# Optimization experiments

Measured on AMD Instinct MI355X. Metric: run time of the kernel, lower is better.

Reference implementation:

```python
import jax, jax.numpy as jnp
import numpy as np

D_MODEL = 1024
NUM_HEADS = 16
HEAD_DIM = D_MODEL // NUM_HEADS
SCALE = HEAD_DIM ** -0.5
LN_EPS = 1e-5
Q_EPS = 1e-5


def bit_quant(W):
    # BitNet b1.58 ternary weight quantization with straight-through estimator.
    gamma = jnp.mean(jnp.abs(W))
    Wq = jnp.clip(jnp.round(W / (gamma + Q_EPS)), -1.0, 1.0) * gamma
    return W + jax.lax.stop_gradient(Wq - W)


def layer_norm(x, gamma, beta):
    mu = jnp.mean(x, axis=-1, keepdims=True)
    var = jnp.mean(jnp.square(x - mu), axis=-1, keepdims=True)
    return (x - mu) * jax.lax.rsqrt(var + LN_EPS) * gamma + beta


def setup_inputs() -> dict:
    key = jax.random.key(0)
    ks = jax.random.split(key, 8)
    B, T, T_ctx, C = 4, 1024, 2048, D_MODEL
    w_std = C ** -0.5
    return {
        "x": jax.random.normal(ks[0], (B, T, C), jnp.float32),
        "context": jax.random.normal(ks[1], (B, T_ctx, C), jnp.float32),
        "Wq": jax.random.normal(ks[2], (C, C), jnp.float32) * w_std,
        "bq": jnp.zeros((C,), jnp.float32),
        "Wk": jax.random.normal(ks[3], (C, C), jnp.float32) * w_std,
        "bk": jnp.zeros((C,), jnp.float32),
        "Wv": jax.random.normal(ks[4], (C, C), jnp.float32) * w_std,
        "bv": jnp.zeros((C,), jnp.float32),
        "Wo": jax.random.normal(ks[5], (C, C), jnp.float32) * w_std,
        "bo": jnp.zeros((C,), jnp.float32),
        "ln_gamma": jnp.ones((C,), jnp.float32),
        "ln_beta": jnp.zeros((C,), jnp.float32),
    }


def reference(x, context, Wq, bq, Wk, bk, Wv, bv, Wo, bo, ln_gamma, ln_beta):
    B, T, C = x.shape
    T_ctx = context.shape[1]
    residual = x
    xn = layer_norm(x, ln_gamma, ln_beta)
    # BitNet-quantized projections (torch Linear: y = x @ W.T + b)
    q = xn @ bit_quant(Wq).T + bq                      # [B,T,C]
    k = context @ bit_quant(Wk).T + bk                 # [B,T_ctx,C]
    v = context @ bit_quant(Wv).T + bv                 # [B,T_ctx,C]
    q = q.reshape(B, T, NUM_HEADS, HEAD_DIM)
    k = k.reshape(B, T_ctx, NUM_HEADS, HEAD_DIM)
    v = v.reshape(B, T_ctx, NUM_HEADS, HEAD_DIM)
    scores = jnp.einsum("bqhd,bkhd->bhqk", q, k) * SCALE   # [B,H,T,T_ctx]
    probs = jax.nn.softmax(scores, axis=-1)
    out = jnp.einsum("bhqk,bkhd->bqhd", probs, v).reshape(B, T, C)
    return residual + (out @ bit_quant(Wo).T + bo)
```

## Files before the change

kernel.cpp:

```cpp
#include <hip/hip_runtime.h>
#include <hip/hip_bf16.h>

typedef __attribute__((ext_vector_type(8))) short s8x;
typedef __attribute__((ext_vector_type(4))) float f4x;
typedef unsigned short u16;
typedef unsigned int u32;

#define T_ 1024
#define TC_ 2048
#define SCLOG2E 0.1803368801111243f

__device__ __forceinline__ u16 f2bf(float f) {
    u32 u = __float_as_uint(f);
    return (u16)((u + 0x7fffu + ((u >> 16) & 1u)) >> 16);
}

#if defined(__has_builtin)
#if __has_builtin(__builtin_amdgcn_cvt_pk_bf16_f32)
#define HAVE_PK 1
#endif
#endif

__device__ __forceinline__ u32 pack2bf(float a, float b) {
#ifdef HAVE_PK
    typedef __attribute__((ext_vector_type(2))) __bf16 bf2t;
    bf2t r = __builtin_amdgcn_cvt_pk_bf16_f32(a, b);
    u32 u;
    __builtin_memcpy(&u, &r, 4);
    return u;
#else
    return (u32)f2bf(a) | ((u32)f2bf(b) << 16);
#endif
}

__device__ __forceinline__ void gload16(const void* g, void* l) {
    __builtin_amdgcn_global_load_lds((const __attribute__((address_space(1))) u32*)g,
                                     (__attribute__((address_space(3))) u32*)l, 16, 0, 0);
}

__global__ __launch_bounds__(256) void absmean_k(const float* __restrict__ W0, const float* __restrict__ W1,
                                                 const float* __restrict__ W2, const float* __restrict__ W3,
                                                 float* __restrict__ gsum) {
    int wi = blockIdx.y;
    const float* W = (wi == 0) ? W0 : (wi == 1) ? W1 : (wi == 2) ? W2 : W3;
    const int n4 = (1024 * 1024) / 4;
    float s = 0.f;
    int stride = gridDim.x * blockDim.x;
    for (int i = blockIdx.x * blockDim.x + threadIdx.x; i < n4; i += stride) {
        float4 v = ((const float4*)W)[i];
        s += fabsf(v.x) + fabsf(v.y) + fabsf(v.z) + fabsf(v.w);
    }
#pragma unroll
    for (int off = 32; off; off >>= 1) s += __shfl_down(s, off, 64);
    __shared__ float ps[4];
    if ((threadIdx.x & 63) == 0) ps[threadIdx.x >> 6] = s;
    __syncthreads();
    if (threadIdx.x == 0) atomicAdd(gsum + wi, ps[0] + ps[1] + ps[2] + ps[3]);
}

__global__ __launch_bounds__(256) void prep_k(
        const float* __restrict__ x, const float* __restrict__ lng, const float* __restrict__ lnb,
        u16* __restrict__ xn,
        const float* __restrict__ ctx, u16* __restrict__ ctxb,
        const float* __restrict__ W0, const float* __restrict__ W1,
        const float* __restrict__ W2, const float* __restrict__ W3,
        u16* __restrict__ D0, u16* __restrict__ D1, u16* __restrict__ D2, u16* __restrict__ D3,
        const float* __restrict__ gsum) {
    __shared__ float ps[8];
    int bx = blockIdx.x, t = threadIdx.x;
    if (bx < 4096) {
        int row = bx;
        float4 xv = ((const float4*)(x + (long)row * 1024))[t];
        float s = xv.x + xv.y + xv.z + xv.w;
        float s2 = xv.x * xv.x + xv.y * xv.y + xv.z * xv.z + xv.w * xv.w;
#pragma unroll
        for (int off = 32; off; off >>= 1) { s += __shfl_down(s, off, 64); s2 += __shfl_down(s2, off, 64); }
        if ((t & 63) == 0) { ps[t >> 6] = s; ps[4 + (t >> 6)] = s2; }
        __syncthreads();
        float S = ps[0] + ps[1] + ps[2] + ps[3];
        float S2 = ps[4] + ps[5] + ps[6] + ps[7];
        float mu = S * (1.f / 1024.f);
        float var = S2 * (1.f / 1024.f) - mu * mu;
        float rstd = rsqrtf(var + 1e-5f);
        float4 gv = ((const float4*)lng)[t];
        float4 bv = ((const float4*)lnb)[t];
        uint2 o;
        o.x = pack2bf((xv.x - mu) * rstd * gv.x + bv.x, (xv.y - mu) * rstd * gv.y + bv.y);
        o.y = pack2bf((xv.z - mu) * rstd * gv.z + bv.z, (xv.w - mu) * rstd * gv.w + bv.w);
        ((uint2*)(xn + (long)row * 1024))[t] = o;
    } else if (bx < 12288) {
        int i = (bx - 4096) * 256 + t;
        float4 v = ((const float4*)ctx)[i];
        uint2 o = {pack2bf(v.x, v.y), pack2bf(v.z, v.w)};
        ((uint2*)ctxb)[i] = o;
    } else {
        int wi = (bx - 12288) >> 10;
        const float* W = (wi == 0) ? W0 : (wi == 1) ? W1 : (wi == 2) ? W2 : W3;
        u16* D = (wi == 0) ? D0 : (wi == 1) ? D1 : (wi == 2) ? D2 : D3;
        float inv = 1.0f / (gsum[wi] * (1.0f / 1048576.0f) + 1e-5f);
        int i = ((bx - 12288) & 1023) * 256 + t;
        float4 wv = ((const float4*)W)[i];
        uint2 o;
        o.x = pack2bf(fminf(1.f, fmaxf(-1.f, rintf(wv.x * inv))),
                      fminf(1.f, fmaxf(-1.f, rintf(wv.y * inv))));
        o.y = pack2bf(fminf(1.f, fmaxf(-1.f, rintf(wv.z * inv))),
                      fminf(1.f, fmaxf(-1.f, rintf(wv.w * inv))));
        ((uint2*)D)[i] = o;
    }
}

__global__ __launch_bounds__(256) void gemm_fused(
        const u16* __restrict__ xn, const u16* __restrict__ ctxb,
        const u16* __restrict__ wtq, const u16* __restrict__ wtk, const u16* __restrict__ wtv,
        const float* __restrict__ bq, const float* __restrict__ bk, const float* __restrict__ bv,
        const float* __restrict__ gsum,
        u16* __restrict__ qb, u16* __restrict__ kb, u16* __restrict__ vtb) {
    __shared__ __align__(16) char smem[32768];
    int tid = threadIdx.x;
    int w = tid >> 6, l = tid & 63, lq = l & 15, lh = l >> 4;
    int wm = (w >> 1) * 64, wn = (w & 1) * 64;
    int bx = blockIdx.x;
    int xcd = bx & 7;
    int prob, m0, n0, gidx;
    const u16 *A, *Wt;
    const float* bias;
    float sc;
    if (bx < 256) {
        int local = bx >> 3;
        prob = 0; A = xn; Wt = wtq; bias = bq; sc = SCLOG2E; gidx = 0;
        m0 = (xcd * 4 + (local & 3)) * 128;
        n0 = (local >> 2) * 128;
    } else {
        int b = bx - 256;
        int local3 = b >> 3;
        int kv = local3 & 1;
        int idx = local3 >> 1;
        prob = 1 + kv; A = ctxb;
        Wt = kv ? wtv : wtk; bias = kv ? bv : bk; sc = 1.0f; gidx = 1 + kv;
        m0 = (xcd * 8 + (idx & 7)) * 128;
        n0 = (idx >> 3) * 128;
    }
    char* AsB = smem;
    char* BsB = smem + 16384;
    f4x acc[4][4] = {};
    int rb = tid >> 3;
    int cg = (tid & 7) ^ (rb & 7);
    const u16* Ag = A + (long)m0 * 1024 + cg * 8;
    const u16* Bg = Wt + (long)n0 * 1024 + cg * 8;
    for (int k0 = 0; k0 < 1024; k0 += 64) {
        __syncthreads();
#pragma unroll
        for (int i = 0; i < 4; i++) {
            gload16(Ag + (long)(i * 32 + rb) * 1024 + k0, AsB + (i * 256 + tid) * 16);
            gload16(Bg + (long)(i * 32 + rb) * 1024 + k0, BsB + (i * 256 + tid) * 16);
        }
        __syncthreads();
#pragma unroll
        for (int s = 0; s < 2; s++) {
            int sl = (s * 4 + lh) ^ (lq & 7);
            s8x af[4], bfr[4];
#pragma unroll
            for (int i = 0; i < 4; i++) {
                af[i] = *(const s8x*)(AsB + (wm + i * 16 + lq) * 128 + sl * 16);
                bfr[i] = *(const s8x*)(BsB + (wn + i * 16 + lq) * 128 + sl * 16);
            }
#pragma unroll
            for (int i = 0; i < 4; i++)
#pragma unroll
                for (int j = 0; j < 4; j++)
                    acc[i][j] = __builtin_amdgcn_mfma_f32_16x16x32_bf16(af[i], bfr[j], acc[i][j], 0, 0, 0);
        }
    }
    float gamma = gsum[gidx] * (1.0f / 1048576.0f) * sc;
    if (prob < 2) {
        u16* outq = (prob == 0) ? qb : kb;
        int tshift = (prob == 0) ? 10 : 11;
        int tmask = (1 << tshift) - 1;
#pragma unroll
        for (int i = 0; i < 4; i++) {
            int gr = m0 + wm + i * 16 + lh * 4;
#pragma unroll
            for (int j = 0; j < 4; j++) {
                int gc = n0 + wn + j * 16 + lq;
                float bb = bias[gc] * sc;
                int h = gc >> 6, d = gc & 63;
#pragma unroll
                for (int r = 0; r < 4; r++) {
                    int row = gr + r;
                    int bidx = row >> tshift, tt = row & tmask;
                    outq[((((long)(bidx * 16 + h)) << tshift) + tt) * 64 + d] = f2bf(acc[i][j][r] * gamma + bb);
                }
            }
        }
    } else {
        __syncthreads();
        char* Ct = smem;
#pragma unroll
        for (int i = 0; i < 4; i++) {
            int tt = wm + i * 16 + lh * 4;
#pragma unroll
            for (int j = 0; j < 4; j++) {
                int c = wn + j * 16 + lq;
                float bb = bias[n0 + c];
                uint2 pk;
                pk.x = pack2bf(acc[i][j][0] * gamma + bb, acc[i][j][1] * gamma + bb);
                pk.y = pack2bf(acc[i][j][2] * gamma + bb, acc[i][j][3] * gamma + bb);
                int slot = (tt >> 3) ^ (c & 15);
                *(uint2*)(Ct + c * 256 + slot * 16 + (tt & 7) * 2) = pk;
            }
        }
        __syncthreads();
        int bb2 = m0 >> 11, t0 = m0 & 2047;
#pragma unroll
        for (int it = 0; it < 8; it++) {
            int e = it * 256 + tid;
            int c = e >> 4, ch = e & 15;
            int slot = ch ^ (c & 15);
            s8x v = *(const s8x*)(Ct + c * 256 + slot * 16);
            int gcg = n0 + c;
            int h = gcg >> 6, d = gcg & 63;
            *(s8x*)(vtb + ((long)((bb2 * 16 + h) * 64 + d)) * TC_ + t0 + ch * 8) = v;
        }
    }
}

__global__ __launch_bounds__(256) void gemm_o(const u16* __restrict__ A, const u16* __restrict__ Wt,
                                              const float* __restrict__ bias, const float* __restrict__ gsum,
                                              const float* __restrict__ residual, float* __restrict__ outr) {
    __shared__ __align__(16) char smem[24576];
    int tid = threadIdx.x;
    int w = tid >> 6, l = tid & 63, lq = l & 15, lh = l >> 4;
    int wm = (w >> 1) * 64, wn = (w & 1) * 32;
    int bx = blockIdx.x;
    int xcd = bx & 7, local = bx >> 3;
    int m0 = (xcd * 4 + (local & 3)) * 128;
    int n0 = (local >> 2) * 64;
    char* AsB = smem;
    char* BsB = smem + 16384;
    f4x acc[4][2] = {};
    int rb = tid >> 3;
    int cg = (tid & 7) ^ (rb & 7);
    const u16* Ag = A + (long)m0 * 1024 + cg * 8;
    const u16* Bg = Wt + (long)n0 * 1024 + cg * 8;
    for (int k0 = 0; k0 < 1024; k0 += 64) {
        __syncthreads();
#pragma unroll
        for (int i = 0; i < 4; i++)
            gload16(Ag + (long)(i * 32 + rb) * 1024 + k0, AsB + (i * 256 + tid) * 16);
#pragma unroll
        for (int i = 0; i < 2; i++)
            gload16(Bg + (long)(i * 32 + rb) * 1024 + k0, BsB + (i * 256 + tid) * 16);
        __syncthreads();
#pragma unroll
        for (int s = 0; s < 2; s++) {
            int sl = (s * 4 + lh) ^ (lq & 7);
            s8x af[4], bfr[2];
#pragma unroll
            for (int i = 0; i < 4; i++)
                af[i] = *(const s8x*)(AsB + (wm + i * 16 + lq) * 128 + sl * 16);
#pragma unroll
            for (int j = 0; j < 2; j++)
                bfr[j] = *(const s8x*)(BsB + (wn + j * 16 + lq) * 128 + sl * 16);
#pragma unroll
            for (int i = 0; i < 4; i++)
#pragma unroll
                for (int j = 0; j < 2; j++)
                    acc[i][j] = __builtin_amdgcn_mfma_f32_16x16x32_bf16(af[i], bfr[j], acc[i][j], 0, 0, 0);
        }
    }
    float gamma = gsum[3] * (1.0f / 1048576.0f);
#pragma unroll
    for (int i = 0; i < 4; i++) {
        int gr = m0 + wm + i * 16 + lh * 4;
#pragma unroll
        for (int j = 0; j < 2; j++) {
            int gc = n0 + wn + j * 16 + lq;
            float bb = bias[gc];
#pragma unroll
            for (int r = 0; r < 4; r++) {
                long idx = (long)(gr + r) * 1024 + gc;
                outr[idx] = residual[idx] + acc[i][j][r] * gamma + bb;
            }
        }
    }
}

__global__ __launch_bounds__(512) void attn_k(const u16* __restrict__ qh, const u16* __restrict__ kh,
                                              const u16* __restrict__ vth,
                                              float* __restrict__ Opart, float* __restrict__ Mpart,
                                              float* __restrict__ Lpart) {
    __shared__ __align__(16) char smem[51200];
    int tid = threadIdx.x, w = tid >> 6, l = tid & 63, lq = l & 15, lh = l >> 4;
    int bh = blockIdx.x, q0 = blockIdx.y * 128, half = blockIdx.z;
    const u16* qp = qh + ((long)bh * T_ + q0) * 64;
    const u16* kp = kh + (long)bh * TC_ * 64 + half * 1024 * 64;
    const u16* vp = vth + (long)bh * 64 * TC_ + half * 1024;
#pragma unroll
    for (int i = 0; i < 2; i++) {
        int cid = i * 512 + tid;
        int r = cid >> 3, c = (cid & 7) ^ (r & 7);
        gload16(qp + r * 64 + c * 8, smem + cid * 16);
    }
    __syncthreads();
    s8x qf0, qf1;
    {
        int qrow = w * 16 + lq;
        qf0 = *(const s8x*)(smem + qrow * 128 + ((lh) ^ (qrow & 7)) * 16);
        qf1 = *(const s8x*)(smem + qrow * 128 + ((4 + lh) ^ (qrow & 7)) * 16);
    }
    __syncthreads();
#define STAGE_KV(kt, buf)                                                      \
    {                                                                          \
        char* Kb = smem + (buf) * 16384;                                       \
        char* Vb = Kb + 8192;                                                  \
        int r = tid >> 3, c = (tid & 7) ^ (r & 7);                             \
        gload16(kp + ((kt) * 64 + r) * 64 + c * 8, Kb + tid * 16);             \
        gload16(vp + (long)r * TC_ + (kt) * 64 + c * 8, Vb + tid * 16);        \
    }
    STAGE_KV(0, 0);
    f4x oacc[4] = {};
    f4x lrun = {};
    float mrun = -1e30f;
    const s8x ones = {16256, 16256, 16256, 16256, 16256, 16256, 16256, 16256};
    char* Psb = smem + 32768 + w * 2304;
    for (int kt = 0; kt < 16; kt++) {
        __syncthreads();
        if (kt + 1 < 16) STAGE_KV(kt + 1, (kt + 1) & 1);
        char* Ksb = smem + (kt & 1) * 16384;
        char* Vsb = Ksb + 8192;
        f4x z[4];
#pragma unroll
        for (int ni = 0; ni < 4; ni++) {
            int kr = ni * 16 + lq;
            s8x a0 = *(const s8x*)(Ksb + kr * 128 + ((lh) ^ (kr & 7)) * 16);
            s8x a1 = *(const s8x*)(Ksb + kr * 128 + ((4 + lh) ^ (kr & 7)) * 16);
            f4x zz = {0.f, 0.f, 0.f, 0.f};
            zz = __builtin_amdgcn_mfma_f32_16x16x32_bf16(a0, qf0, zz, 0, 0, 0);
            zz = __builtin_amdgcn_mfma_f32_16x16x32_bf16(a1, qf1, zz, 0, 0, 0);
            z[ni] = zz;
        }
        float mx = fmaxf(fmaxf(fmaxf(z[0][0], z[0][1]), fmaxf(z[0][2], z[0][3])),
                         fmaxf(fmaxf(z[1][0], z[1][1]), fmaxf(z[1][2], z[1][3])));
        mx = fmaxf(mx, fmaxf(fmaxf(fmaxf(z[2][0], z[2][1]), fmaxf(z[2][2], z[2][3])),
                             fmaxf(fmaxf(z[3][0], z[3][1]), fmaxf(z[3][2], z[3][3]))));
#pragma unroll
        for (int s = 1; s <= 32; s <<= 1) mx = fmaxf(mx, __shfl_xor(mx, s));
        float mn = fmaxf(mrun, mx);
        float al = __builtin_amdgcn_exp2f(mrun - mn);
        mrun = mn;
#pragma unroll
        for (int ni = 0; ni < 4; ni++) {
            uint2 pk;
            pk.x = pack2bf(__builtin_amdgcn_exp2f(z[ni][0] - mn), __builtin_amdgcn_exp2f(z[ni][1] - mn));
            pk.y = pack2bf(__builtin_amdgcn_exp2f(z[ni][2] - mn), __builtin_amdgcn_exp2f(z[ni][3] - mn));
            *(uint2*)(Psb + lq * 144 + ni * 32 + lh * 8) = pk;
        }
        if (al != 1.0f) {
#pragma unroll
            for (int nd = 0; nd < 4; nd++)
#pragma unroll
                for (int r = 0; r < 4; r++) oacc[nd][r] *= al;
#pragma unroll
            for (int r = 0; r < 4; r++) lrun[r] *= al;
        }
        s8x vf0[4], vf1[4];
#pragma unroll
        for (int nd = 0; nd < 4; nd++) {
            int vr = nd * 16 + lq;
            vf0[nd] = *(const s8x*)(Vsb + vr * 128 + ((lh) ^ (vr & 7)) * 16);
            vf1[nd] = *(const s8x*)(Vsb + vr * 128 + ((4 + lh) ^ (vr & 7)) * 16);
        }
        s8x pf0 = *(const s8x*)(Psb + lq * 144 + lh * 16);
        s8x pf1 = *(const s8x*)(Psb + lq * 144 + 64 + lh * 16);
        f4x rs = {0.f, 0.f, 0.f, 0.f};
        rs = __builtin_amdgcn_mfma_f32_16x16x32_bf16(pf0, ones, rs, 0, 0, 0);
        rs = __builtin_amdgcn_mfma_f32_16x16x32_bf16(pf1, ones, rs, 0, 0, 0);
#pragma unroll
        for (int r = 0; r < 4; r++) lrun[r] += rs[r];
#pragma unroll
        for (int nd = 0; nd < 4; nd++) {
            oacc[nd] = __builtin_amdgcn_mfma_f32_16x16x32_bf16(pf0, vf0[nd], oacc[nd], 0, 0, 0);
            oacc[nd] = __builtin_amdgcn_mfma_f32_16x16x32_bf16(pf1, vf1[nd], oacc[nd], 0, 0, 0);
        }
    }
    int pidx = (bh * 8 + blockIdx.y) * 2 + half;
    float* Op = Opart + (long)pidx * 8192;
#pragma unroll
    for (int r = 0; r < 4; r++) {
        int ql = w * 16 + lh * 4 + r;
#pragma unroll
        for (int nd = 0; nd < 4; nd++)
            Op[ql * 64 + nd * 16 + lq] = oacc[nd][r];
        if (lq == 0) Lpart[(long)pidx * 128 + ql] = lrun[r];
    }
    if (l == 0) Mpart[pidx * 8 + w] = mrun;
}

__global__ __launch_bounds__(256) void merge_k(const float* __restrict__ Opart,
                                               const float* __restrict__ Mpart,
                                               const float* __restrict__ Lpart,
                                               u16* __restrict__ attn) {
    int pg = blockIdx.x;
    int bh = pg >> 3, qt = pg & 7;
    int t = threadIdx.x;
    int q = t >> 1, dh = (t & 1) * 32;
    int p0 = pg * 2, p1 = pg * 2 + 1;
    float m0 = Mpart[p0 * 8 + (q >> 4)], m1 = Mpart[p1 * 8 + (q >> 4)];
    float l0 = Lpart[(long)p0 * 128 + q], l1 = Lpart[(long)p1 * 128 + q];
    float M = fmaxf(m0, m1);
    float a0 = __builtin_amdgcn_exp2f(m0 - M);
    float a1 = __builtin_amdgcn_exp2f(m1 - M);
    float rinv = 1.f / (l0 * a0 + l1 * a1);
    a0 *= rinv; a1 *= rinv;
    const float4* O0 = (const float4*)(Opart + (long)p0 * 8192 + q * 64 + dh);
    const float4* O1 = (const float4*)(Opart + (long)p1 * 8192 + q * 64 + dh);
    int b = bh >> 4, h = bh & 15;
    uint2* dst = (uint2*)(attn + ((long)(b * T_ + qt * 128 + q)) * 1024 + h * 64 + dh);
#pragma unroll
    for (int i = 0; i < 8; i++) {
        float4 v0 = O0[i], v1 = O1[i];
        uint2 o;
        o.x = pack2bf(v0.x * a0 + v1.x * a1, v0.y * a0 + v1.y * a1);
        o.y = pack2bf(v0.z * a0 + v1.z * a1, v0.w * a0 + v1.w * a1);
        dst[i] = o;
    }
}

extern "C" void kernel_launch(void* const* d_in, const int* in_sizes, int n_in,
                              void* d_out, int out_size, void* d_ws, size_t ws_size,
                              hipStream_t stream) {
    const float* x   = (const float*)d_in[0];
    const float* ctx = (const float*)d_in[1];
    const float* Wq  = (const float*)d_in[2];
    const float* bq  = (const float*)d_in[3];
    const float* Wk  = (const float*)d_in[4];
    const float* bk  = (const float*)d_in[5];
    const float* Wv  = (const float*)d_in[6];
    const float* bv  = (const float*)d_in[7];
    const float* Wo  = (const float*)d_in[8];
    const float* bo  = (const float*)d_in[9];
    const float* lng = (const float*)d_in[10];
    const float* lnb = (const float*)d_in[11];
    float* out = (float*)d_out;

    char* ws = (char*)d_ws;
    float* gsum = (float*)ws;
    size_t off = 256;
    u16* wtq  = (u16*)(ws + off); off += (size_t)1024 * 1024 * 2;
    u16* wtk  = (u16*)(ws + off); off += (size_t)1024 * 1024 * 2;
    u16* wtv  = (u16*)(ws + off); off += (size_t)1024 * 1024 * 2;
    u16* wto  = (u16*)(ws + off); off += (size_t)1024 * 1024 * 2;
    u16* ctxb = (u16*)(ws + off); off += (size_t)8192 * 1024 * 2;
    u16* xn   = (u16*)(ws + off); off += (size_t)4096 * 1024 * 2;
    u16* qb_  = (u16*)(ws + off); off += (size_t)4096 * 1024 * 2;
    u16* kb   = (u16*)(ws + off); off += (size_t)8192 * 1024 * 2;
    u16* vtb  = (u16*)(ws + off); off += (size_t)8192 * 1024 * 2;
    float* Opart = (float*)(ws + off); off += (size_t)1024 * 8192 * 4;
    float* Mpart = (float*)(ws + off); off += (size_t)1024 * 8 * 4;
    float* Lpart = (float*)(ws + off); off += (size_t)1024 * 128 * 4;
    u16* attnb = xn;

    hipMemsetAsync(gsum, 0, 16, stream);
    absmean_k<<<dim3(128, 4), 256, 0, stream>>>(Wq, Wk, Wv, Wo, gsum);
    prep_k<<<16384, 256, 0, stream>>>(x, lng, lnb, xn, ctx, ctxb,
                                      Wq, Wk, Wv, Wo, wtq, wtk, wtv, wto, gsum);
    gemm_fused<<<1280, 256, 0, stream>>>(xn, ctxb, wtq, wtk, wtv, bq, bk, bv, gsum, qb_, kb, vtb);
    attn_k<<<dim3(64, 8, 2), 512, 0, stream>>>(qb_, kb, vtb, Opart, Mpart, Lpart);
    merge_k<<<512, 256, 0, stream>>>(Opart, Mpart, Lpart, attnb);
    gemm_o<<<512, 256, 0, stream>>>(attnb, wto, bo, gsum, x, out);
}
```

Measured before the change: 282.6 us.

## Double-buffer GEMM k-loop with paired-row swizzle and store attention partials in bf16

Both projection GEMMs switch from a single-buffered 64-wide k step with two barriers per iteration to a double-buffered 32-wide k step. The next tile's global-to-LDS load is issued before the MFMAs on the current tile, leaving one barrier per step, and a new paired-row XOR swizzle with precomputed LDS offsets goes with it. Separately, the attention partial outputs are written as bf16 instead of fp32, which halves that traffic in attn_k and merge_k. The partial buffers now alias dead workspace regions (ctxb, wtq). This trades some precision in the partial sums for less bandwidth, and it relies on those aliased buffers no longer being needed.

```diff
diff --git a/kernel.cpp b/kernel.cpp
--- a/kernel.cpp
+++ b/kernel.cpp
@@ -10,6 +10,7 @@
 #define TC_ 2048
 #define SCLOG2E 0.1803368801111243f
 
+__device__ __forceinline__ float bf2f(u16 u) { return __uint_as_float(((u32)u) << 16); }
 __device__ __forceinline__ u16 f2bf(float f) {
     u32 u = __float_as_uint(f);
     return (u16)((u + 0x7fffu + ((u >> 16) & 1u)) >> 16);
@@ -140,36 +141,47 @@
         m0 = (xcd * 8 + (idx & 7)) * 128;
         n0 = (idx >> 3) * 128;
     }
-    char* AsB = smem;
-    char* BsB = smem + 16384;
+    int sp = tid >> 3, ss = tid & 7;
+    int st = ss ^ (sp & 7);
+    int r0 = sp * 2 + (st >> 2), c0 = st & 3;
+    const u16* Ag = A + (long)(m0 + r0) * 1024 + c0 * 8;
+    const u16* Bg = Wt + (long)(n0 + r0) * 1024 + c0 * 8;
+    int aoff[4], boff[4];
+#pragma unroll
+    for (int i = 0; i < 4; i++) {
+        int ar = wm + i * 16 + lq, ap = ar >> 1;
+        aoff[i] = ap * 128 + (((((ar & 1) << 2) | lh) ^ (ap & 7)) * 16);
+        int br = wn + i * 16 + lq, bp = br >> 1;
+        boff[i] = bp * 128 + (((((br & 1) << 2) | lh) ^ (bp & 7)) * 16);
+    }
     f4x acc[4][4] = {};
-    int rb = tid >> 3;
-    int cg = (tid & 7) ^ (rb & 7);
-    const u16* Ag = A + (long)m0 * 1024 + cg * 8;
-    const u16* Bg = Wt + (long)n0 * 1024 + cg * 8;
-    for (int k0 = 0; k0 < 1024; k0 += 64) {
-        __syncthreads();
+#define STAGE_G(kt, buf)                                                   \
+    {                                                                      \
+        char* Ad = smem + (buf) * 8192;                                    \
+        char* Bd = smem + 16384 + (buf) * 8192;                            \
+        int kk = (kt) * 32;                                                \
+        gload16(Ag + kk, Ad + tid * 16);                                   \
+        gload16(Ag + kk + 64 * 1024, Ad + 4096 + tid * 16);                \
+        gload16(Bg + kk, Bd + tid * 16);                                   \
+        gload16(Bg + kk + 64 * 1024, Bd + 4096 + tid * 16);                \
+    }
+    STAGE_G(0, 0);
+    for (int kt = 0; kt < 32; kt++) {
+        __syncthreads();
+        if (kt + 1 < 32) STAGE_G(kt + 1, (kt + 1) & 1);
+        const char* Ac = smem + (kt & 1) * 8192;
+        const char* Bc = smem + 16384 + (kt & 1) * 8192;
+        s8x af[4], bfr[4];
 #pragma unroll
         for (int i = 0; i < 4; i++) {
-            gload16(Ag + (long)(i * 32 + rb) * 1024 + k0, AsB + (i * 256 + tid) * 16);
-            gload16(Bg + (long)(i * 32 + rb) * 1024 + k0, BsB + (i * 256 + tid) * 16);
-        }
-        __syncthreads();
-#pragma unroll
-        for (int s = 0; s < 2; s++) {
-            int sl = (s * 4 + lh) ^ (lq & 7);
-            s8x af[4], bfr[4];
-#pragma unroll
-            for (int i = 0; i < 4; i++) {
-                af[i] = *(const s8x*)(AsB + (wm + i * 16 + lq) * 128 + sl * 16);
-                bfr[i] = *(const s8x*)(BsB + (wn + i * 16 + lq) * 128 + sl * 16);
-            }
-#pragma unroll
-            for (int i = 0; i < 4; i++)
-#pragma unroll
-                for (int j = 0; j < 4; j++)
-                    acc[i][j] = __builtin_amdgcn_mfma_f32_16x16x32_bf16(af[i], bfr[j], acc[i][j], 0, 0, 0);
-        }
+            af[i] = *(const s8x*)(Ac + aoff[i]);
+            bfr[i] = *(const s8x*)(Bc + boff[i]);
+        }
+#pragma unroll
+        for (int i = 0; i < 4; i++)
+#pragma unroll
+            for (int j = 0; j < 4; j++)
+                acc[i][j] = __builtin_amdgcn_mfma_f32_16x16x32_bf16(af[i], bfr[j], acc[i][j], 0, 0, 0);
     }
     float gamma = gsum[gidx] * (1.0f / 1048576.0f) * sc;
     if (prob < 2) {
@@ -235,38 +247,48 @@
     int xcd = bx & 7, local = bx >> 3;
     int m0 = (xcd * 4 + (local & 3)) * 128;
     int n0 = (local >> 2) * 64;
-    char* AsB = smem;
-    char* BsB = smem + 16384;
+    int sp = tid >> 3, ss = tid & 7;
+    int st = ss ^ (sp & 7);
+    int r0 = sp * 2 + (st >> 2), c0 = st & 3;
+    const u16* Ag = A + (long)(m0 + r0) * 1024 + c0 * 8;
+    const u16* Bg = Wt + (long)(n0 + r0) * 1024 + c0 * 8;
+    int aoff[4], boff[2];
+#pragma unroll
+    for (int i = 0; i < 4; i++) {
+        int ar = wm + i * 16 + lq, ap = ar >> 1;
+        aoff[i] = ap * 128 + (((((ar & 1) << 2) | lh) ^ (ap & 7)) * 16);
+    }
+#pragma unroll
+    for (int j = 0; j < 2; j++) {
+        int br = wn + j * 16 + lq, bp = br >> 1;
+        boff[j] = bp * 128 + (((((br & 1) << 2) | lh) ^ (bp & 7)) * 16);
+    }
     f4x acc[4][2] = {};
-    int rb = tid >> 3;
-    int cg = (tid & 7) ^ (rb & 7);
-    const u16* Ag = A + (long)m0 * 1024 + cg * 8;
-    const u16* Bg = Wt + (long)n0 * 1024 + cg * 8;
-    for (int k0 = 0; k0 < 1024; k0 += 64) {
-        __syncthreads();
+#define STAGE_O(kt, buf)                                                   \
+    {                                                                      \
+        char* Ad = smem + (buf) * 8192;                                    \
+        char* Bd = smem + 16384 + (buf) * 4096;                            \
+        int kk = (kt) * 32;                                                \
+        gload16(Ag + kk, Ad + tid * 16);                                   \
+        gload16(Ag + kk + 64 * 1024, Ad + 4096 + tid * 16);                \
+        gload16(Bg + kk, Bd + tid * 16);                                   \
+    }
+    STAGE_O(0, 0);
+    for (int kt = 0; kt < 32; kt++) {
+        __syncthreads();
+        if (kt + 1 < 32) STAGE_O(kt + 1, (kt + 1) & 1);
+        const char* Ac = smem + (kt & 1) * 8192;
+        const char* Bc = smem + 16384 + (kt & 1) * 4096;
+        s8x af[4], bfr[2];
+#pragma unroll
+        for (int i = 0; i < 4; i++) af[i] = *(const s8x*)(Ac + aoff[i]);
+#pragma unroll
+        for (int j = 0; j < 2; j++) bfr[j] = *(const s8x*)(Bc + boff[j]);
 #pragma unroll
         for (int i = 0; i < 4; i++)
-            gload16(Ag + (long)(i * 32 + rb) * 1024 + k0, AsB + (i * 256 + tid) * 16);
-#pragma unroll
-        for (int i = 0; i < 2; i++)
-            gload16(Bg + (long)(i * 32 + rb) * 1024 + k0, BsB + (i * 256 + tid) * 16);
-        __syncthreads();
-#pragma unroll
-        for (int s = 0; s < 2; s++) {
-            int sl = (s * 4 + lh) ^ (lq & 7);
-            s8x af[4], bfr[2];
-#pragma unroll
-            for (int i = 0; i < 4; i++)
-                af[i] = *(const s8x*)(AsB + (wm + i * 16 + lq) * 128 + sl * 16);
 #pragma unroll
             for (int j = 0; j < 2; j++)
-                bfr[j] = *(const s8x*)(BsB + (wn + j * 16 + lq) * 128 + sl * 16);
-#pragma unroll
-            for (int i = 0; i < 4; i++)
-#pragma unroll
-                for (int j = 0; j < 2; j++)
-                    acc[i][j] = __builtin_amdgcn_mfma_f32_16x16x32_bf16(af[i], bfr[j], acc[i][j], 0, 0, 0);
-        }
+                acc[i][j] = __builtin_amdgcn_mfma_f32_16x16x32_bf16(af[i], bfr[j], acc[i][j], 0, 0, 0);
     }
     float gamma = gsum[3] * (1.0f / 1048576.0f);
 #pragma unroll
@@ -287,7 +309,7 @@
 
 __global__ __launch_bounds__(512) void attn_k(const u16* __restrict__ qh, const u16* __restrict__ kh,
                                               const u16* __restrict__ vth,
-                                              float* __restrict__ Opart, float* __restrict__ Mpart,
+                                              u16* __restrict__ Opart, float* __restrict__ Mpart,
                                               float* __restrict__ Lpart) {
     __shared__ __align__(16) char smem[51200];
     int tid = threadIdx.x, w = tid >> 6, l = tid & 63, lq = l & 15, lh = l >> 4;
@@ -384,19 +406,19 @@
         }
     }
     int pidx = (bh * 8 + blockIdx.y) * 2 + half;
-    float* Op = Opart + (long)pidx * 8192;
+    u16* Op = Opart + (long)pidx * 8192;
 #pragma unroll
     for (int r = 0; r < 4; r++) {
         int ql = w * 16 + lh * 4 + r;
 #pragma unroll
         for (int nd = 0; nd < 4; nd++)
-            Op[ql * 64 + nd * 16 + lq] = oacc[nd][r];
+            Op[ql * 64 + nd * 16 + lq] = f2bf(oacc[nd][r]);
         if (lq == 0) Lpart[(long)pidx * 128 + ql] = lrun[r];
     }
     if (l == 0) Mpart[pidx * 8 + w] = mrun;
 }
 
-__global__ __launch_bounds__(256) void merge_k(const float* __restrict__ Opart,
+__global__ __launch_bounds__(256) void merge_k(const u16* __restrict__ Opart,
                                                const float* __restrict__ Mpart,
                                                const float* __restrict__ Lpart,
                                                u16* __restrict__ attn) {
@@ -412,16 +434,18 @@
     float a1 = __builtin_amdgcn_exp2f(m1 - M);
     float rinv = 1.f / (l0 * a0 + l1 * a1);
     a0 *= rinv; a1 *= rinv;
-    const float4* O0 = (const float4*)(Opart + (long)p0 * 8192 + q * 64 + dh);
-    const float4* O1 = (const float4*)(Opart + (long)p1 * 8192 + q * 64 + dh);
+    const uint2* O0 = (const uint2*)(Opart + (long)p0 * 8192 + q * 64 + dh);
+    const uint2* O1 = (const uint2*)(Opart + (long)p1 * 8192 + q * 64 + dh);
     int b = bh >> 4, h = bh & 15;
     uint2* dst = (uint2*)(attn + ((long)(b * T_ + qt * 128 + q)) * 1024 + h * 64 + dh);
 #pragma unroll
     for (int i = 0; i < 8; i++) {
-        float4 v0 = O0[i], v1 = O1[i];
+        uint2 v0 = O0[i], v1 = O1[i];
         uint2 o;
-        o.x = pack2bf(v0.x * a0 + v1.x * a1, v0.y * a0 + v1.y * a1);
-        o.y = pack2bf(v0.z * a0 + v1.z * a1, v0.w * a0 + v1.w * a1);
+        o.x = pack2bf(bf2f((u16)v0.x) * a0 + bf2f((u16)v1.x) * a1,
+                      bf2f((u16)(v0.x >> 16)) * a0 + bf2f((u16)(v1.x >> 16)) * a1);
+        o.y = pack2bf(bf2f((u16)v0.y) * a0 + bf2f((u16)v1.y) * a1,
+                      bf2f((u16)(v0.y >> 16)) * a0 + bf2f((u16)(v1.y >> 16)) * a1);
         dst[i] = o;
     }
 }
@@ -455,10 +479,10 @@
     u16* qb_  = (u16*)(ws + off); off += (size_t)4096 * 1024 * 2;
     u16* kb   = (u16*)(ws + off); off += (size_t)8192 * 1024 * 2;
     u16* vtb  = (u16*)(ws + off); off += (size_t)8192 * 1024 * 2;
-    float* Opart = (float*)(ws + off); off += (size_t)1024 * 8192 * 4;
-    float* Mpart = (float*)(ws + off); off += (size_t)1024 * 8 * 4;
-    float* Lpart = (float*)(ws + off); off += (size_t)1024 * 128 * 4;
     u16* attnb = xn;
+    u16* Opart = ctxb;
+    float* Mpart = (float*)wtq;
+    float* Lpart = (float*)((char*)wtq + 32768);
 
     hipMemsetAsync(gsum, 0, 16, stream);
     absmean_k<<<dim3(128, 4), 256, 0, stream>>>(Wq, Wk, Wv, Wo, gsum);
```

After: 280.5 us. Within noise of the previous version (-0.7%).
